# Kernel optimization log

Hardware: AMD Instinct MI355X
Metric: run time of the kernel (lower is better)

Reference implementation:

```python
import jax, jax.numpy as jnp
import numpy as np

N_CELLS = 50000


def setup_inputs() -> dict:
    key = jax.random.key(0)
    ks = jax.random.split(key, 8)
    in_dim, emb = 1000, 128
    sl0 = 1.0 / np.sqrt(in_dim)
    sl1 = 1.0 / np.sqrt(emb)
    return {
        "x": jax.random.normal(ks[0], (in_dim, N_CELLS), dtype=jnp.float32),
        "knn_edge_index": jax.random.randint(ks[1], (2, 800000), 0, N_CELLS, dtype=jnp.int64),
        "W_l0": jax.random.normal(ks[2], (emb, in_dim), dtype=jnp.float32) * sl0,
        "b_l0": jnp.zeros((emb,), dtype=jnp.float32),
        "W_r0": jax.random.normal(ks[3], (emb, in_dim), dtype=jnp.float32) * sl0,
        "W_l1": jax.random.normal(ks[4], (emb, emb), dtype=jnp.float32) * sl1,
        "b_l1": jnp.zeros((emb,), dtype=jnp.float32),
        "W_r1": jax.random.normal(ks[5], (emb, emb), dtype=jnp.float32) * sl1,
    }


def _sage_layer(h, src, dst, W_l, b_l, W_r, n_nodes):
    # mean aggregation of source-node features onto target nodes (PyG SAGEConv default)
    agg = jax.ops.segment_sum(h[src], dst, num_segments=n_nodes)      # [N, d_in]
    cnt = jax.ops.segment_sum(jnp.ones((src.shape[0],), h.dtype), dst,
                              num_segments=n_nodes)                   # [N]
    mean_nbr = agg / jnp.maximum(cnt, 1.0)[:, None]
    out = mean_nbr @ W_l.T + b_l + h @ W_r.T                          # [N, d_out]
    return jax.nn.elu(out)  # dropout is identity in eval mode


def reference(x, knn_edge_index, W_l0, b_l0, W_r0, W_l1, b_l1, W_r1):
    src, dst = knn_edge_index[0], knn_edge_index[1]
    h = x.T                                            # (num_cells, num_genes)
    n = h.shape[0]
    h = _sage_layer(h, src, dst, W_l0, b_l0, W_r0, n)
    h = _sage_layer(h, src, dst, W_l1, b_l1, W_r1, n)
    return h
```

## Files before the change

kernel.cpp:

```cpp
#include <hip/hip_runtime.h>
#include <hip/hip_bf16.h>


#define IN_DIM 1000

typedef __attribute__((ext_vector_type(8))) short bf16x8;
typedef __attribute__((ext_vector_type(4))) float f32x4;

static __device__ __forceinline__ unsigned int f2bf(float f){
  union { float f; unsigned int u; } v; v.f = f;
  return (v.u + 0x7fffu + ((v.u >> 16) & 1u)) >> 16;
}
static __device__ __forceinline__ float bl(unsigned v){
  union { unsigned u; float f; } t; t.u = v << 16; return t.f;
}
static __device__ __forceinline__ float bh(unsigned v){
  union { unsigned u; float f; } t; t.u = v & 0xFFFF0000u; return t.f;
}
static __device__ __forceinline__ void glds16(const void* g, void* lds){
  __builtin_amdgcn_global_load_lds(
      (const __attribute__((address_space(1))) unsigned int*)g,
      (__attribute__((address_space(3))) unsigned int*)lds, 16, 0, 0);
}

__global__ void prep_k(const float* __restrict__ Wl0, const float* __restrict__ Wr0,
                       const float* __restrict__ Wl1, const float* __restrict__ Wr1,
                       unsigned short* __restrict__ img0,
                       unsigned short* __restrict__ img1, int total0, int total1){
  int idx = blockIdx.x*256 + threadIdx.x;
  if (idx < total0){
    int j  = idx & 7;
    int l  = (idx >> 3) & 63;
    int ks = (idx >> 9) & 1;
    int n  = (idx >> 10) & 3;
    int w  = (idx >> 12) & 3;
    int s  = idx >> 14;
    int row = w*64 + n*16 + (l & 15);
    int k   = s*64 + ks*32 + (l >> 4)*8 + j;
    float val = 0.f;
    if (k < IN_DIM)
      val = (row < 128) ? Wl0[(size_t)row*IN_DIM + k] : Wr0[(size_t)(row-128)*IN_DIM + k];
    img0[idx] = (unsigned short)f2bf(val);
    return;
  }
  idx -= total0;
  if (idx >= total1) return;
  int s   = idx / (256*72);
  int rem = idx % (256*72);
  int n   = rem / 72;
  int e   = rem % 72;
  float val = 0.f;
  if (e < 64){
    int k = s*64 + e;
    if (k < 128) val = (n < 128) ? Wl1[(size_t)n*128 + k] : Wr1[(size_t)(n-128)*128 + k];
  }
  img1[idx] = (unsigned short)f2bf(val);
}

__global__ void scan1_k(const int* __restrict__ cnt, int* __restrict__ rowp,
                        float* __restrict__ inv, int* __restrict__ bsum,
                        int* __restrict__ ticket, int N, int nb){
  __shared__ int wt[4];
  __shared__ int lastS;
  int bid = blockIdx.x;
  int i = bid*256 + threadIdx.x;
  int lane = threadIdx.x & 63, wid = threadIdx.x >> 6;
  int v = (i < N) ? cnt[i] : 0;
  int sc = v;
  #pragma unroll
  for (int off = 1; off < 64; off <<= 1){
    int o = __shfl_up(sc, off);
    if (lane >= off) sc += o;
  }
  if (lane == 63) wt[wid] = sc;
  __syncthreads();
  if (threadIdx.x == 0){
    int a = 0;
    #pragma unroll
    for (int j = 0; j < 4; ++j){ int t = wt[j]; wt[j] = a; a += t; }
    bsum[bid] = a;
    if (bid == nb-1 && (N & 255)) rowp[N] = a;
  }
  __syncthreads();
  if (i < N){
    rowp[i] = wt[wid] + sc - v;
    inv[i]  = 1.0f / fmaxf((float)v, 1.0f);
  }
  __threadfence();
  if (threadIdx.x == 0){
    int t = __hip_atomic_fetch_add(ticket, 1, __ATOMIC_ACQ_REL, __HIP_MEMORY_SCOPE_AGENT);
    lastS = (t == (int)gridDim.x - 1);
  }
  __syncthreads();
  if (lastS){
    __threadfence();
    int t2 = threadIdx.x;
    int bv = (t2 < nb) ? __hip_atomic_load(&bsum[t2], __ATOMIC_RELAXED,
                                           __HIP_MEMORY_SCOPE_AGENT) : 0;
    int sc2 = bv;
    #pragma unroll
    for (int off = 1; off < 64; off <<= 1){
      int o = __shfl_up(sc2, off);
      if (lane >= off) sc2 += o;
    }
    __syncthreads();
    if (lane == 63) wt[wid] = sc2;
    __syncthreads();
    if (t2 == 0){
      int a = 0;
      #pragma unroll
      for (int j = 0; j < 4; ++j){ int t = wt[j]; wt[j] = a; a += t; }
      bsum[nb] = a;
      if (!(N & 255)) rowp[N] = 0;
    }
    __syncthreads();
    if (t2 < nb) bsum[t2] = wt[wid] + sc2 - bv;
  }
}

__global__ void fill_col_k(const int* __restrict__ ei, int E,
                           const int* __restrict__ rowp, const int* __restrict__ bsum,
                           int* __restrict__ pos, int* __restrict__ col){
  int e = blockIdx.x*blockDim.x + threadIdx.x;
  if (e < E){
    int src = ei[e];
    int dst = ei[(size_t)E + e];
    int p = atomicAdd(&pos[dst], 1);
    col[rowp[dst] + bsum[dst >> 8] + p] = src;
  }
}

__global__ __launch_bounds__(256, 3) void gemm0_count_k(
    const float* __restrict__ x, const unsigned short* __restrict__ B0img,
    unsigned short* __restrict__ ybl, unsigned short* __restrict__ ybr,
    int N, int Ka, int nsteps, int nblk,
    const int* __restrict__ ei, int E, int* __restrict__ cnt){
  if ((int)blockIdx.x >= nblk){
    int idx = ((int)blockIdx.x - nblk)*256 + threadIdx.x;
    if (idx < E) atomicAdd(&cnt[ei[(size_t)E + idx]], 1);
    return;
  }
  __shared__ char AsB[64*144];
  const int tid = threadIdx.x;
  const int c0  = blockIdx.x * 64;
  const int l   = tid & 63, wid = tid >> 6;
  const int nw  = wid * 64;
  const int lr  = l & 15, lq = l >> 4;
  const int c2  = (tid & 31)*2;
  const int kg  = tid >> 5;
  const int ceff = ((c0 + c2) < N) ? (c0 + c2) : 0;

  f32x4 acc[4][4];
  #pragma unroll
  for (int m=0;m<4;++m)
    #pragma unroll
    for (int n=0;n<4;++n) acc[m][n] = (f32x4){0.f,0.f,0.f,0.f};

  const char* bbase = (const char*)B0img + (size_t)wid*8192 + (size_t)l*16;

  float2 xv[8];
  bf16x8 bf[8];

  auto loadx = [&](int step){
    #pragma unroll
    for (int kk = 0; kk < 8; ++kk){
      int k = step*64 + kg*8 + kk;
      k = (k < Ka) ? k : (Ka - 1);
      xv[kk] = *(const float2*)&x[(size_t)k*N + ceff];
    }
  };
  auto loadB = [&](int s){
    const char* p = bbase + (size_t)s*32768;
    #pragma unroll
    for (int n = 0; n < 4; ++n)
      #pragma unroll
      for (int ks = 0; ks < 2; ++ks)
        bf[n*2+ks] = *(const bf16x8*)(p + n*2048 + ks*1024);
  };
  auto packx = [&](){
    unsigned w0[4], w1[4];
    #pragma unroll
    for (int j = 0; j < 4; ++j){
      asm("v_cvt_pk_bf16_f32 %0, %1, %2" : "=v"(w0[j]) : "v"(xv[2*j].x), "v"(xv[2*j+1].x));
      asm("v_cvt_pk_bf16_f32 %0, %1, %2" : "=v"(w1[j]) : "v"(xv[2*j].y), "v"(xv[2*j+1].y));
    }
    *(uint4*)&AsB[(c2+0)*144 + kg*16] = make_uint4(w0[0],w0[1],w0[2],w0[3]);
    *(uint4*)&AsB[(c2+1)*144 + kg*16] = make_uint4(w1[0],w1[1],w1[2],w1[3]);
  };

  loadx(0);
  for (int s = 0; s < nsteps; ++s){
    if (s) __syncthreads();
    loadB(s);
    packx();
    if (s+1 < nsteps) loadx(s+1);
    __syncthreads();
    #pragma unroll
    for (int ks = 0; ks < 2; ++ks){
      bf16x8 a[4];
      #pragma unroll
      for (int m = 0; m < 4; ++m)
        a[m] = *(const bf16x8*)&AsB[(m*16 + lr)*144 + ks*64 + lq*16];
      #pragma unroll
      for (int n = 0; n < 4; ++n)
        #pragma unroll
        for (int m = 0; m < 4; ++m)
          acc[m][n] = __builtin_amdgcn_mfma_f32_16x16x32_bf16(a[m], bf[n*2+ks], acc[m][n], 0, 0, 0);
    }
  }
  unsigned short* op = (nw < 128) ? ybl : ybr;
  const int       nc = (nw < 128) ? nw : nw - 128;
  #pragma unroll
  for (int m = 0; m < 4; ++m){
    int rbase = c0 + m*16 + lq*4;
    #pragma unroll
    for (int q = 0; q < 4; ++q){
      int r = rbase + q;
      if (r < N){
        #pragma unroll
        for (int n = 0; n < 4; ++n)
          op[(size_t)r*128 + nc + n*16 + lr] = (unsigned short)f2bf(acc[m][n][q]);
      }
    }
  }
}

__global__ __launch_bounds__(256, 3) void gemm1_k(
    const void* __restrict__ Ap, const unsigned short* __restrict__ Bimg,
    unsigned short* __restrict__ ybl, unsigned short* __restrict__ ybr,
    int N, int nsteps){
  __shared__ char AsB[64*128];
  __shared__ char BsB[36864];
  const int tid = threadIdx.x;
  const int c0  = blockIdx.x * 64;
  const int l   = tid & 63, wid = tid >> 6;
  const int nw  = wid * 64;
  const int lr  = l & 15, lq = l >> 4;

  f32x4 acc[4][4];
  #pragma unroll
  for (int m=0;m<4;++m)
    #pragma unroll
    for (int n=0;n<4;++n) acc[m][n] = (f32x4){0.f,0.f,0.f,0.f};

  const char* h1b = (const char*)Ap;

  for (int s = 0; s < nsteps; ++s){
    if (s) __syncthreads();
    {
      const char* bsrc = (const char*)Bimg + (size_t)s*36864;
      #pragma unroll
      for (int i = 0; i < 9; ++i){
        int chunk = i*256 + tid;
        glds16(bsrc + (size_t)chunk*16, &BsB[(i*256 + wid*64)*16]);
      }
    }
    #pragma unroll
    for (int i = 0; i < 2; ++i){
      int chunk = i*256 + tid;
      int row = chunk >> 3, cb = (chunk & 7)*16;
      glds16(h1b + (size_t)(c0 + row)*256 + s*128 + cb,
             &AsB[(i*256 + wid*64)*16]);
    }
    __syncthreads();
    #pragma unroll
    for (int ks = 0; ks < 2; ++ks){
      bf16x8 a[4];
      #pragma unroll
      for (int m = 0; m < 4; ++m){
        int row = m*16 + lr;
        int colb = (ks*64 + lq*16) ^ ((row & 7) << 4);
        a[m] = *(const bf16x8*)&AsB[row*128 + colb];
      }
      #pragma unroll
      for (int n = 0; n < 4; ++n){
        bf16x8 b = *(const bf16x8*)&BsB[(nw + n*16 + lr)*144 + ks*64 + lq*16];
        #pragma unroll
        for (int m = 0; m < 4; ++m)
          acc[m][n] = __builtin_amdgcn_mfma_f32_16x16x32_bf16(a[m], b, acc[m][n], 0, 0, 0);
      }
    }
  }
  unsigned short* op  = (nw < 128) ? ybl : ybr;
  const int       nc  = (nw < 128) ? nw : nw - 128;
  #pragma unroll
  for (int m = 0; m < 4; ++m){
    int rbase = c0 + m*16 + lq*4;
    #pragma unroll
    for (int q = 0; q < 4; ++q){
      int r = rbase + q;
      if (r < N){
        #pragma unroll
        for (int n = 0; n < 4; ++n)
          op[(size_t)r*128 + nc + n*16 + lr] = (unsigned short)f2bf(acc[m][n][q]);
      }
    }
  }
}

template<int LAYER>
__global__ void aggregate_k(const unsigned short* __restrict__ ybl,
    const unsigned short* __restrict__ ybr,
    const int* __restrict__ rowp, const int* __restrict__ bsum,
    const int* __restrict__ col,
    const float* __restrict__ inv, const float* __restrict__ bias,
    void* __restrict__ outp, int N){
  int node = blockIdx.x*4 + (threadIdx.x >> 6);
  int l = threadIdx.x & 63;
  if (node >= N) return;
  int b = rowp[node]   + bsum[node >> 8];
  int e = rowp[node+1] + bsum[(node+1) >> 8];
  int f2 = l*2;
  const unsigned* yl = (const unsigned*)ybl;
  float s0=0.f,s1=0.f,t0=0.f,t1=0.f,u0=0.f,u1=0.f,w0=0.f,w1=0.f;
  for (int k = b; k < e; k += 8){
    unsigned a[8];
    #pragma unroll
    for (int j = 0; j < 8; ++j){
      int kj = k + j;
      int idx = col[(kj < e) ? kj : b];
      unsigned v = yl[(size_t)idx*64 + l];
      a[j] = (kj < e) ? v : 0u;
    }
    s0 += bl(a[0]); s1 += bh(a[0]); t0 += bl(a[1]); t1 += bh(a[1]);
    u0 += bl(a[2]); u1 += bh(a[2]); w0 += bl(a[3]); w1 += bh(a[3]);
    s0 += bl(a[4]); s1 += bh(a[4]); t0 += bl(a[5]); t1 += bh(a[5]);
    u0 += bl(a[6]); u1 += bh(a[6]); w0 += bl(a[7]); w1 += bh(a[7]);
  }
  s0 = (s0 + t0) + (u0 + w0);
  s1 = (s1 + t1) + (u1 + w1);
  unsigned vs = *(const unsigned*)&ybr[(size_t)node*128 + f2];
  float iv = inv[node];
  float r0 = s0*iv + bias[f2]   + bl(vs);
  float r1 = s1*iv + bias[f2+1] + bh(vs);
  r0 = (r0 > 0.f) ? r0 : expm1f(r0);
  r1 = (r1 > 0.f) ? r1 : expm1f(r1);
  if (LAYER == 0){
    int sf = f2 >> 6, fo = f2 & 63, g = fo >> 3;
    size_t byte = (size_t)node*256 + (size_t)(sf*128 + ((g ^ (node & 7)) << 4) + (fo & 7)*2);
    *(unsigned*)((char*)outp + byte) = f2bf(r0) | (f2bf(r1) << 16);
  } else {
    *(float2*)((float*)outp + (size_t)node*128 + f2) = make_float2(r0, r1);
  }
}

static inline size_t align_up(size_t v, size_t a){ return (v + a - 1) & ~(a - 1); }

extern "C" void kernel_launch(void* const* d_in, const int* in_sizes, int n_in,
                              void* d_out, int out_size, void* d_ws, size_t ws_size,
                              hipStream_t stream) {
  const float* x   = (const float*)d_in[0];
  const int*   ei  = (const int*)d_in[1];
  const float* Wl0 = (const float*)d_in[2];
  const float* bl0 = (const float*)d_in[3];
  const float* Wr0 = (const float*)d_in[4];
  const float* Wl1 = (const float*)d_in[5];
  const float* bl1 = (const float*)d_in[6];
  const float* Wr1 = (const float*)d_in[7];

  int N = in_sizes[0] / IN_DIM;
  int E = in_sizes[1] / 2;

  const int NS0 = 16;
  const int NS1 = 2;
  int nsb = (N + 255) / 256;

  char* base = (char*)d_ws;
  size_t off = 0;
  unsigned short* ybl = (unsigned short*)(base + off); off = align_up(off + (size_t)N*128*2, 256);
  unsigned short* ybr = (unsigned short*)(base + off); off = align_up(off + (size_t)N*128*2, 256);
  float* inv  = (float*)(base + off); off = align_up(off + (size_t)N*4, 256);
  int*   cnt  = (int*)  (base + off); off = align_up(off + (size_t)N*8 + 256, 256);
  int*   pos  = cnt + N;
  int*   ticket = cnt + 2*N;
  int*   rowp = (int*)  (base + off); off = align_up(off + (size_t)(N+1)*4, 256);
  int*   bsum = (int*)  (base + off); off = align_up(off + (size_t)(nsb+1)*4, 256);
  int*   col  = (int*)  (base + off); off = align_up(off + (size_t)E*4, 256);
  unsigned short* B0img = (unsigned short*)(base + off); off = align_up(off + (size_t)524288*2, 256);
  unsigned short* B1img = (unsigned short*)(base + off); off = align_up(off + (size_t)NS1*18432*2, 256);
  void* h1b = d_out;
  (void)ws_size; (void)n_in; (void)out_size;

  hipMemsetAsync(cnt, 0, (size_t)N*8 + 256, stream);

  int t0n = 524288, t1n = NS1*18432;
  prep_k<<<(t0n+t1n+255)/256, 256, 0, stream>>>(Wl0, Wr0, Wl1, Wr1,
                                                B0img, B1img, t0n, t1n);

  int nblk = (N + 63) / 64;
  int cblk = (E + 255) / 256;
  int ablk = (N + 3) / 4;

  gemm0_count_k<<<nblk + cblk, 256, 0, stream>>>(x, B0img, ybl, ybr, N, IN_DIM,
                                                 NS0, nblk, ei, E, cnt);
  scan1_k<<<nsb, 256, 0, stream>>>(cnt, rowp, inv, bsum, ticket, N, nsb);
  fill_col_k<<<(E+255)/256, 256, 0, stream>>>(ei, E, rowp, bsum, pos, col);
  aggregate_k<0><<<ablk, 256, 0, stream>>>(ybl, ybr, rowp, bsum, col, inv, bl0, h1b, N);

  gemm1_k<<<nblk, 256, 0, stream>>>(h1b, B1img, ybl, ybr, N, NS1);
  aggregate_k<1><<<ablk, 256, 0, stream>>>(ybl, ybr, rowp, bsum, col, inv, bl1, d_out, N);
}
```

Baseline: 238.6 us.

## Double-buffer gemm0 LDS tiles and interleave edge-count blocks with GEMM blocks

The layer-0 GEMM kernel now keeps two LDS tiles and two register sets for the x and weight fragments. This lets it prefetch two steps ahead, and each k-step needs one barrier instead of two. The grid is also remapped so the edge-count blocks are spread between the GEMM blocks rather than queued after them, which aims to overlap the atomic counting with the memory-bound GEMM. The launch-bounds occupancy hint drops from 3 to 2 to make room for the extra registers. The cost is more register and LDS pressure, which may reduce the number of resident blocks.

```diff
diff --git a/kernel.cpp b/kernel.cpp
--- a/kernel.cpp
+++ b/kernel.cpp
@@ -130,19 +130,24 @@
   }
 }
 
-__global__ __launch_bounds__(256, 3) void gemm0_count_k(
+__global__ __launch_bounds__(256, 2) void gemm0_count_k(
     const float* __restrict__ x, const unsigned short* __restrict__ B0img,
     unsigned short* __restrict__ ybl, unsigned short* __restrict__ ybr,
     int N, int Ka, int nsteps, int nblk,
     const int* __restrict__ ei, int E, int* __restrict__ cnt){
-  if ((int)blockIdx.x >= nblk){
-    int idx = ((int)blockIdx.x - nblk)*256 + threadIdx.x;
+  const int bid = (int)blockIdx.x;
+  int S = (int)gridDim.x / nblk; if (S < 1) S = 1;
+  const int g = bid / S, r = bid - g*S;
+  if (!(r == 0 && g < nblk)){
+    int gemmBefore = (bid + S - 1) / S;
+    if (gemmBefore > nblk) gemmBefore = nblk;
+    int idx = (bid - gemmBefore)*256 + threadIdx.x;
     if (idx < E) atomicAdd(&cnt[ei[(size_t)E + idx]], 1);
     return;
   }
-  __shared__ char AsB[64*144];
+  __shared__ char AsB[2][64*144];
   const int tid = threadIdx.x;
-  const int c0  = blockIdx.x * 64;
+  const int c0  = g * 64;
   const int l   = tid & 63, wid = tid >> 6;
   const int nw  = wid * 64;
   const int lr  = l & 15, lq = l >> 4;
@@ -158,10 +163,10 @@
 
   const char* bbase = (const char*)B0img + (size_t)wid*8192 + (size_t)l*16;
 
-  float2 xv[8];
-  bf16x8 bf[8];
-
-  auto loadx = [&](int step){
+  float2 xva[8], xvb[8];
+  bf16x8 bfa[8], bfb[8];
+
+  auto loadx = [&](int step, float2* xv){
     #pragma unroll
     for (int kk = 0; kk < 8; ++kk){
       int k = step*64 + kg*8 + kk;
@@ -169,7 +174,7 @@
       xv[kk] = *(const float2*)&x[(size_t)k*N + ceff];
     }
   };
-  auto loadB = [&](int s){
+  auto loadB = [&](int s, bf16x8* bf){
     const char* p = bbase + (size_t)s*32768;
     #pragma unroll
     for (int n = 0; n < 4; ++n)
@@ -177,37 +182,50 @@
       for (int ks = 0; ks < 2; ++ks)
         bf[n*2+ks] = *(const bf16x8*)(p + n*2048 + ks*1024);
   };
-  auto packx = [&](){
+  auto packx = [&](const float2* xv, char* As){
     unsigned w0[4], w1[4];
     #pragma unroll
     for (int j = 0; j < 4; ++j){
       asm("v_cvt_pk_bf16_f32 %0, %1, %2" : "=v"(w0[j]) : "v"(xv[2*j].x), "v"(xv[2*j+1].x));
       asm("v_cvt_pk_bf16_f32 %0, %1, %2" : "=v"(w1[j]) : "v"(xv[2*j].y), "v"(xv[2*j+1].y));
     }
-    *(uint4*)&AsB[(c2+0)*144 + kg*16] = make_uint4(w0[0],w0[1],w0[2],w0[3]);
-    *(uint4*)&AsB[(c2+1)*144 + kg*16] = make_uint4(w1[0],w1[1],w1[2],w1[3]);
+    *(uint4*)&As[(c2+0)*144 + kg*16] = make_uint4(w0[0],w0[1],w0[2],w0[3]);
+    *(uint4*)&As[(c2+1)*144 + kg*16] = make_uint4(w1[0],w1[1],w1[2],w1[3]);
   };
-
-  loadx(0);
-  for (int s = 0; s < nsteps; ++s){
-    if (s) __syncthreads();
-    loadB(s);
-    packx();
-    if (s+1 < nsteps) loadx(s+1);
-    __syncthreads();
+  auto domfma = [&](const char* As, const bf16x8* bf){
     #pragma unroll
     for (int ks = 0; ks < 2; ++ks){
       bf16x8 a[4];
       #pragma unroll
       for (int m = 0; m < 4; ++m)
-        a[m] = *(const bf16x8*)&AsB[(m*16 + lr)*144 + ks*64 + lq*16];
+        a[m] = *(const bf16x8*)&As[(m*16 + lr)*144 + ks*64 + lq*16];
       #pragma unroll
       for (int n = 0; n < 4; ++n)
         #pragma unroll
         for (int m = 0; m < 4; ++m)
           acc[m][n] = __builtin_amdgcn_mfma_f32_16x16x32_bf16(a[m], bf[n*2+ks], acc[m][n], 0, 0, 0);
     }
-  }
+  };
+
+  loadx(0, xva);
+  loadB(0, bfa);
+  loadx(1, xvb);
+
+  for (int s = 0; s < nsteps; s += 2){
+    packx(xva, AsB[0]);
+    if (s + 2 < nsteps) loadx(s + 2, xva);
+    if (s + 1 < nsteps) loadB(s + 1, bfb);
+    __syncthreads();
+    domfma(AsB[0], bfa);
+    if (s + 1 < nsteps){
+      packx(xvb, AsB[1]);
+      if (s + 3 < nsteps) loadx(s + 3, xvb);
+      if (s + 2 < nsteps) loadB(s + 2, bfa);
+      __syncthreads();
+      domfma(AsB[1], bfb);
+    }
+  }
+
   unsigned short* op = (nw < 128) ? ybl : ybr;
   const int       nc = (nw < 128) ? nw : nw - 128;
   #pragma unroll
@@ -215,11 +233,11 @@
     int rbase = c0 + m*16 + lq*4;
     #pragma unroll
     for (int q = 0; q < 4; ++q){
-      int r = rbase + q;
-      if (r < N){
+      int r2 = rbase + q;
+      if (r2 < N){
         #pragma unroll
         for (int n = 0; n < 4; ++n)
-          op[(size_t)r*128 + nc + n*16 + lr] = (unsigned short)f2bf(acc[m][n][q]);
+          op[(size_t)r2*128 + nc + n*16 + lr] = (unsigned short)f2bf(acc[m][n][q]);
       }
     }
   }
```

Result: slower. 344.1 us (+44.2%).
